# Kernel optimization log

Measured on AMD Instinct MI355X. Metric: run time of the kernel, lower is better.

The kernel has to match this reference:

```python
import jax, jax.numpy as jnp
import numpy as np

N_NODES = 100000
N_EDGES = 1600000
D = 64        # atom_embed_dim
EF = 4        # edge_feat_dim
V = 100       # num_elements


def setup_inputs() -> dict:
    key = jax.random.key(0)
    ks = jax.random.split(key, 10)
    x_ids = jax.random.randint(ks[0], (N_NODES,), 0, V, dtype=jnp.int64 if jax.config.jax_enable_x64 else jnp.int32)
    edge_index = jax.random.randint(ks[1], (2, N_EDGES), 0, N_NODES, dtype=jnp.int64 if jax.config.jax_enable_x64 else jnp.int32)
    edge_attr = jax.random.normal(ks[2], (N_EDGES, EF), dtype=jnp.float32)
    emb = jax.random.normal(ks[3], (V, D), dtype=jnp.float32)
    s_in = 1.0 / np.sqrt(D + EF)
    s_d = 1.0 / np.sqrt(D)
    W1 = jax.random.uniform(ks[4], (D, D + EF), jnp.float32, -s_in, s_in)
    b1 = jax.random.uniform(ks[5], (D,), jnp.float32, -s_in, s_in)
    Wu1 = jax.random.uniform(ks[6], (D, D), jnp.float32, -s_d, s_d)
    bu1 = jax.random.uniform(ks[7], (D,), jnp.float32, -s_d, s_d)
    W2 = jax.random.uniform(ks[8], (D, D + EF), jnp.float32, -s_in, s_in)
    b2 = jax.random.uniform(ks[9], (D,), jnp.float32, -s_in, s_in)
    k2 = jax.random.split(jax.random.key(1), 2)
    Wu2 = jax.random.uniform(k2[0], (D, D), jnp.float32, -s_d, s_d)
    bu2 = jax.random.uniform(k2[1], (D,), jnp.float32, -s_d, s_d)
    return {"x_ids": x_ids, "edge_index": edge_index, "edge_attr": edge_attr,
            "emb": emb, "W1": W1, "b1": b1, "Wu1": Wu1, "bu1": bu1,
            "W2": W2, "b2": b2, "Wu2": Wu2, "bu2": bu2}


def _round(x, src, dst, edge_attr, Wm, bm, Wu, bu):
    # gather src node feats, concat edge feats, msg MLP, scatter-add to dst
    m = jnp.concatenate([x[src], edge_attr], axis=-1)       # (E, D+EF)
    m = jax.nn.relu(m @ Wm.T + bm)                           # (E, D)
    agg = jax.ops.segment_sum(m, dst, num_segments=x.shape[0])  # (N, D)
    return jax.nn.relu((x + agg) @ Wu.T + bu)                # (N, D)


def reference(x_ids, edge_index, edge_attr, emb, W1, b1, Wu1, bu1, W2, b2, Wu2, bu2):
    src, dst = edge_index[0], edge_index[1]
    x = emb[x_ids]                                           # (N, D)
    x = _round(x, src, dst, edge_attr, W1, b1, Wu1, bu1)
    x = _round(x, src, dst, edge_attr, W2, b2, Wu2, bu2)
    return x.mean(axis=0)                                    # (D,)
```

## Files before the change

### kernel.cpp

```cpp
#include <hip/hip_runtime.h>

#define DD    64
#define WCOLS 68

__device__ __forceinline__ float lane_bcast(float v, int k) {
    return __int_as_float(__builtin_amdgcn_readlane(__float_as_int(v), k));
}

__global__ __launch_bounds__(256) void hist_kernel(
    const int* __restrict__ dst, int* __restrict__ deg, int E)
{
    int i = blockIdx.x * 256 + threadIdx.x;
    int stride = gridDim.x * 256;
    for (; i < E; i += stride) atomicAdd(&deg[dst[i]], 1);
}

__global__ __launch_bounds__(256) void scan1_kernel(
    const int* __restrict__ deg, int* __restrict__ rowp, int* __restrict__ bsum, int N)
{
    __shared__ int lds[256];
    int base = blockIdx.x * 1024;
    int t = threadIdx.x;
    int idx0 = base + t * 4;
    int v[4];
    #pragma unroll
    for (int j = 0; j < 4; ++j) v[j] = (idx0 + j < N) ? deg[idx0 + j] : 0;
    lds[t] = v[0] + v[1] + v[2] + v[3];
    __syncthreads();
    for (int off = 1; off < 256; off <<= 1) {
        int x = (t >= off) ? lds[t - off] : 0;
        __syncthreads();
        lds[t] += x;
        __syncthreads();
    }
    int run = (t > 0) ? lds[t - 1] : 0;
    if (t == 255) bsum[blockIdx.x] = lds[255];
    #pragma unroll
    for (int j = 0; j < 4; ++j) {
        if (idx0 + j < N) rowp[idx0 + j] = run;
        run += v[j];
    }
}

__global__ __launch_bounds__(256) void scan2_kernel(int* __restrict__ bsum, int nchunks)
{
    __shared__ int lds[256];
    int t = threadIdx.x;
    int v = (t < nchunks) ? bsum[t] : 0;
    lds[t] = v;
    __syncthreads();
    for (int off = 1; off < 256; off <<= 1) {
        int x = (t >= off) ? lds[t - off] : 0;
        __syncthreads();
        lds[t] += x;
        __syncthreads();
    }
    if (t < nchunks) bsum[t] = (t > 0) ? lds[t - 1] : 0;
}

__global__ __launch_bounds__(256) void scan3_kernel(
    int* __restrict__ rowp, const int* __restrict__ bsum, int* __restrict__ cursor,
    int N, int E)
{
    int i = blockIdx.x * 256 + threadIdx.x;
    if (i == 0) rowp[N] = E;
    if (i < N) {
        int v = rowp[i] + bsum[i >> 10];
        rowp[i] = v;
        cursor[i] = v;
    }
}

__global__ __launch_bounds__(256) void fill_kernel(
    const int* __restrict__ src, const int* __restrict__ dst,
    const float* __restrict__ eattr, int* __restrict__ cursor,
    int* __restrict__ srcp, float4* __restrict__ eap, int E)
{
    int i = blockIdx.x * 256 + threadIdx.x;
    int stride = gridDim.x * 256;
    for (; i < E; i += stride) {
        int d = dst[i];
        int pos = atomicAdd(&cursor[d], 1);
        srcp[pos] = src[i];
        eap[pos] = *(const float4*)(eattr + (size_t)i * 4);
    }
}

__global__ __launch_bounds__(256) void init_kernel(
    const int* __restrict__ x_ids, const float* __restrict__ emb,
    const float* __restrict__ W1, const float* __restrict__ b1,
    float* __restrict__ x0, float* __restrict__ Y, int N)
{
    __shared__ float WaT[64 * 64];
    for (int i = threadIdx.x; i < 64 * 64; i += 256) {
        int d = i & 63, k = i >> 6;
        WaT[i] = W1[d * WCOLS + k];
    }
    __syncthreads();

    int lane = threadIdx.x & 63;
    int wid  = (blockIdx.x * 256 + threadIdx.x) >> 6;
    int nw   = (gridDim.x * 256) >> 6;
    float bias = b1[lane];

    for (int base = wid * 4; base < N; base += nw * 4) {
        int nvalid = N - base; if (nvalid > 4) nvalid = 4;
        float xv[4], acc[4];
        #pragma unroll
        for (int j = 0; j < 4; ++j) {
            xv[j] = (j < nvalid) ? emb[x_ids[base + j] * DD + lane] : 0.f;
            acc[j] = bias;
        }
        #pragma unroll 8
        for (int k = 0; k < 64; ++k) {
            float w = WaT[k * 64 + lane];
            #pragma unroll
            for (int j = 0; j < 4; ++j)
                acc[j] = fmaf(w, lane_bcast(xv[j], k), acc[j]);
        }
        #pragma unroll
        for (int j = 0; j < 4; ++j) {
            if (j < nvalid) {
                size_t o = (size_t)(base + j) * DD + lane;
                x0[o] = xv[j];
                Y[o]  = acc[j];
            }
        }
    }
}

template<bool FUSE_Y, bool FINAL>
__global__ __launch_bounds__(256) void fused_kernel(
    const int* __restrict__ rowp, const int* __restrict__ srcp,
    const float4* __restrict__ eap, const float* __restrict__ Y_in,
    const float* __restrict__ Wm,
    const float* __restrict__ Wu, const float* __restrict__ bu,
    const float* __restrict__ Wn, const float* __restrict__ bn,
    float* __restrict__ x_io, float* __restrict__ Y_out,
    float* __restrict__ out_mean, int N, float inv_n)
{
    __shared__ float WuT[64 * 64];
    __shared__ float WnT[FUSE_Y ? 64 * 64 : 1];
    __shared__ float red[FINAL ? 256 : 1];
    for (int i = threadIdx.x; i < 64 * 64; i += 256) {
        int d = i & 63, k = i >> 6;
        WuT[i] = Wu[d * DD + k];
        if (FUSE_Y) WnT[i] = Wn[d * WCOLS + k];
    }
    __syncthreads();

    int lane = threadIdx.x & 63;
    int wid  = __builtin_amdgcn_readfirstlane((blockIdx.x * 256 + (int)threadIdx.x) >> 6);
    int nw   = (gridDim.x * 256) >> 6;
    float w0 = Wm[lane * WCOLS + 64];
    float w1 = Wm[lane * WCOLS + 65];
    float w2 = Wm[lane * WCOLS + 66];
    float w3 = Wm[lane * WCOLS + 67];
    float biasu = bu[lane];
    float biasn = FUSE_Y ? bn[lane] : 0.f;
    float lsum = 0.f;

    for (int n = wid; n < N; n += nw) {
        int beg = rowp[n], end = rowp[n + 1];
        float acc = 0.f;
        int e = beg;
        for (; e + 3 < end; e += 4) {
            int s0 = srcp[e], s1 = srcp[e + 1], s2 = srcp[e + 2], s3 = srcp[e + 3];
            float4 a0 = eap[e], a1 = eap[e + 1], a2 = eap[e + 2], a3 = eap[e + 3];
            float y0 = Y_in[(size_t)s0 * DD + lane];
            float y1 = Y_in[(size_t)s1 * DD + lane];
            float y2 = Y_in[(size_t)s2 * DD + lane];
            float y3 = Y_in[(size_t)s3 * DD + lane];
            float m0 = y0 + w0 * a0.x + w1 * a0.y + w2 * a0.z + w3 * a0.w;
            float m1 = y1 + w0 * a1.x + w1 * a1.y + w2 * a1.z + w3 * a1.w;
            float m2 = y2 + w0 * a2.x + w1 * a2.y + w2 * a2.z + w3 * a2.w;
            float m3 = y3 + w0 * a3.x + w1 * a3.y + w2 * a3.z + w3 * a3.w;
            acc += fmaxf(m0, 0.f) + fmaxf(m1, 0.f) + fmaxf(m2, 0.f) + fmaxf(m3, 0.f);
        }
        for (; e < end; ++e) {
            int s0 = srcp[e];
            float4 a0 = eap[e];
            float y0 = Y_in[(size_t)s0 * DD + lane];
            float m0 = y0 + w0 * a0.x + w1 * a0.y + w2 * a0.z + w3 * a0.w;
            acc += fmaxf(m0, 0.f);
        }

        size_t o = (size_t)n * DD + lane;
        float v = x_io[o] + acc;
        float au = biasu;
        #pragma unroll 8
        for (int k = 0; k < 64; ++k)
            au = fmaf(WuT[k * 64 + lane], lane_bcast(v, k), au);
        float oo = fmaxf(au, 0.f);

        if (FUSE_Y) {
            float an = biasn;
            #pragma unroll 8
            for (int k = 0; k < 64; ++k)
                an = fmaf(WnT[k * 64 + lane], lane_bcast(oo, k), an);
            x_io[o]  = oo;
            Y_out[o] = an;
        }
        if (FINAL) lsum += oo;
    }

    if (FINAL) {
        red[threadIdx.x] = lsum;
        __syncthreads();
        if (threadIdx.x < 64) {
            float s = red[threadIdx.x] + red[threadIdx.x + 64] +
                      red[threadIdx.x + 128] + red[threadIdx.x + 192];
            unsafeAtomicAdd(&out_mean[threadIdx.x], s * inv_n);
        }
    }
}

extern "C" void kernel_launch(void* const* d_in, const int* in_sizes, int n_in,
                              void* d_out, int out_size, void* d_ws, size_t ws_size,
                              hipStream_t stream) {
    const int*   x_ids = (const int*)d_in[0];
    const int*   ei    = (const int*)d_in[1];
    const float* eattr = (const float*)d_in[2];
    const float* emb   = (const float*)d_in[3];
    const float* W1    = (const float*)d_in[4];
    const float* b1    = (const float*)d_in[5];
    const float* Wu1   = (const float*)d_in[6];
    const float* bu1   = (const float*)d_in[7];
    const float* W2    = (const float*)d_in[8];
    const float* b2    = (const float*)d_in[9];
    const float* Wu2   = (const float*)d_in[10];
    const float* bu2   = (const float*)d_in[11];

    const int N = in_sizes[0];
    const int E = in_sizes[1] / 2;
    const int* src = ei;
    const int* dst = ei + E;

    float* ws = (float*)d_ws;
    size_t stride = (size_t)N * DD;
    float*  x    = ws;
    float*  Ya   = ws + stride;
    float*  Yb   = ws + 2 * stride;
    float*  eapf = ws + 3 * stride;
    int*    srcp = (int*)(eapf + (size_t)E * 4);
    int*    rowp = srcp + E;
    int*    deg  = rowp + N + 1;
    int*    cur  = deg + N;
    int*    bsum = cur + N;
    float4* eap  = (float4*)eapf;

    float* out = (float*)d_out;
    float inv_n = 1.0f / (float)N;
    int nchunks = (N + 1023) / 1024;

    hipMemsetAsync(deg, 0, (size_t)N * sizeof(int), stream);
    hipMemsetAsync(out, 0, DD * sizeof(float), stream);

    hist_kernel <<<2048, 256, 0, stream>>>(dst, deg, E);
    scan1_kernel<<<nchunks, 256, 0, stream>>>(deg, rowp, bsum, N);
    scan2_kernel<<<1, 256, 0, stream>>>(bsum, nchunks);
    scan3_kernel<<<(N + 255) / 256, 256, 0, stream>>>(rowp, bsum, cur, N, E);
    fill_kernel <<<2048, 256, 0, stream>>>(src, dst, eattr, cur, srcp, eap, E);

    init_kernel<<<1024, 256, 0, stream>>>(x_ids, emb, W1, b1, x, Ya, N);

    fused_kernel<true, false><<<2048, 256, 0, stream>>>(
        rowp, srcp, eap, Ya, W1, Wu1, bu1, W2, b2, x, Yb, nullptr, N, inv_n);
    fused_kernel<false, true><<<2048, 256, 0, stream>>>(
        rowp, srcp, eap, Yb, W2, Wu2, bu2, nullptr, nullptr, x, nullptr, out, N, inv_n);
}
```

Measured before the change: 609.1 us.

## Tile nodes per block with edge-balanced waves and LDS atomic aggregation

Replaces the one-wave-per-node CSR loop with blocks that own 64 consecutive destination nodes. The block's edge range is split evenly across its four waves, and messages are accumulated into a shared-memory tile with LDS float atomics. A per-edge byte holding the local destination index is stored during the fill step. The node update then batches four nodes per wave in the dense matvec to reuse weight loads. This targets load imbalance and per-node loop overhead, at the cost of LDS atomics, an extra byte array, and fewer larger blocks (~1563).

```diff
diff --git a/kernel.cpp b/kernel.cpp
--- a/kernel.cpp
+++ b/kernel.cpp
@@ -2,6 +2,7 @@
 
 #define DD    64
 #define WCOLS 68
+#define TILE  64
 
 __device__ __forceinline__ float lane_bcast(float v, int k) {
     return __int_as_float(__builtin_amdgcn_readlane(__float_as_int(v), k));
@@ -74,15 +75,17 @@
 __global__ __launch_bounds__(256) void fill_kernel(
     const int* __restrict__ src, const int* __restrict__ dst,
     const float* __restrict__ eattr, int* __restrict__ cursor,
-    int* __restrict__ srcp, float4* __restrict__ eap, int E)
+    int* __restrict__ srcp, float4* __restrict__ eap,
+    unsigned char* __restrict__ dstp8, int E)
 {
     int i = blockIdx.x * 256 + threadIdx.x;
     int stride = gridDim.x * 256;
     for (; i < E; i += stride) {
         int d = dst[i];
         int pos = atomicAdd(&cursor[d], 1);
-        srcp[pos] = src[i];
-        eap[pos] = *(const float4*)(eattr + (size_t)i * 4);
+        srcp[pos]  = src[i];
+        eap[pos]   = *(const float4*)(eattr + (size_t)i * 4);
+        dstp8[pos] = (unsigned char)(d & (TILE - 1));
     }
 }
 
@@ -130,78 +133,133 @@
 }
 
 template<bool FUSE_Y, bool FINAL>
-__global__ __launch_bounds__(256) void fused_kernel(
+__global__ __launch_bounds__(256) void tile_kernel(
     const int* __restrict__ rowp, const int* __restrict__ srcp,
-    const float4* __restrict__ eap, const float* __restrict__ Y_in,
-    const float* __restrict__ Wm,
+    const float4* __restrict__ eap, const unsigned char* __restrict__ dstp8,
+    const float* __restrict__ Y_in, const float* __restrict__ Wm,
     const float* __restrict__ Wu, const float* __restrict__ bu,
     const float* __restrict__ Wn, const float* __restrict__ bn,
     float* __restrict__ x_io, float* __restrict__ Y_out,
     float* __restrict__ out_mean, int N, float inv_n)
 {
+    __shared__ float agg[TILE * 64];
     __shared__ float WuT[64 * 64];
     __shared__ float WnT[FUSE_Y ? 64 * 64 : 1];
     __shared__ float red[FINAL ? 256 : 1];
+
     for (int i = threadIdx.x; i < 64 * 64; i += 256) {
         int d = i & 63, k = i >> 6;
+        agg[i] = 0.f;
         WuT[i] = Wu[d * DD + k];
         if (FUSE_Y) WnT[i] = Wn[d * WCOLS + k];
     }
     __syncthreads();
 
     int lane = threadIdx.x & 63;
-    int wid  = __builtin_amdgcn_readfirstlane((blockIdx.x * 256 + (int)threadIdx.x) >> 6);
-    int nw   = (gridDim.x * 256) >> 6;
+    int wv   = __builtin_amdgcn_readfirstlane(threadIdx.x >> 6);
     float w0 = Wm[lane * WCOLS + 64];
     float w1 = Wm[lane * WCOLS + 65];
     float w2 = Wm[lane * WCOLS + 66];
     float w3 = Wm[lane * WCOLS + 67];
+
+    int base = blockIdx.x * TILE;
+    int nend = base + TILE; if (nend > N) nend = N;
+    int beg = rowp[base], end = rowp[nend];
+
+    int T   = end - beg;
+    int per = (T + 3) >> 2;
+    int e0  = beg + wv * per;
+    int e1  = e0 + per; if (e1 > end) e1 = end;
+
+    int e = e0;
+    for (; e + 7 < e1; e += 8) {
+        int s[8]; float4 a[8]; int t8[8];
+        #pragma unroll
+        for (int j = 0; j < 8; ++j) {
+            s[j]  = srcp[e + j];
+            a[j]  = eap[e + j];
+            t8[j] = dstp8[e + j];
+        }
+        float y[8];
+        #pragma unroll
+        for (int j = 0; j < 8; ++j)
+            y[j] = Y_in[(size_t)s[j] * DD + lane];
+        #pragma unroll
+        for (int j = 0; j < 8; ++j) {
+            float m = fmaf(w0, a[j].x, y[j]);
+            m = fmaf(w1, a[j].y, m);
+            m = fmaf(w2, a[j].z, m);
+            m = fmaf(w3, a[j].w, m);
+            m = fmaxf(m, 0.f);
+            atomicAdd(&agg[t8[j] * 64 + lane], m);
+        }
+    }
+    for (; e < e1; ++e) {
+        int s0 = srcp[e];
+        float4 a0 = eap[e];
+        int t0 = dstp8[e];
+        float m = fmaf(w0, a0.x, Y_in[(size_t)s0 * DD + lane]);
+        m = fmaf(w1, a0.y, m);
+        m = fmaf(w2, a0.z, m);
+        m = fmaf(w3, a0.w, m);
+        atomicAdd(&agg[t0 * 64 + lane], fmaxf(m, 0.f));
+    }
+    __syncthreads();
+
     float biasu = bu[lane];
     float biasn = FUSE_Y ? bn[lane] : 0.f;
     float lsum = 0.f;
 
-    for (int n = wid; n < N; n += nw) {
-        int beg = rowp[n], end = rowp[n + 1];
-        float acc = 0.f;
-        int e = beg;
-        for (; e + 3 < end; e += 4) {
-            int s0 = srcp[e], s1 = srcp[e + 1], s2 = srcp[e + 2], s3 = srcp[e + 3];
-            float4 a0 = eap[e], a1 = eap[e + 1], a2 = eap[e + 2], a3 = eap[e + 3];
-            float y0 = Y_in[(size_t)s0 * DD + lane];
-            float y1 = Y_in[(size_t)s1 * DD + lane];
-            float y2 = Y_in[(size_t)s2 * DD + lane];
-            float y3 = Y_in[(size_t)s3 * DD + lane];
-            float m0 = y0 + w0 * a0.x + w1 * a0.y + w2 * a0.z + w3 * a0.w;
-            float m1 = y1 + w0 * a1.x + w1 * a1.y + w2 * a1.z + w3 * a1.w;
-            float m2 = y2 + w0 * a2.x + w1 * a2.y + w2 * a2.z + w3 * a2.w;
-            float m3 = y3 + w0 * a3.x + w1 * a3.y + w2 * a3.z + w3 * a3.w;
-            acc += fmaxf(m0, 0.f) + fmaxf(m1, 0.f) + fmaxf(m2, 0.f) + fmaxf(m3, 0.f);
-        }
-        for (; e < end; ++e) {
-            int s0 = srcp[e];
-            float4 a0 = eap[e];
-            float y0 = Y_in[(size_t)s0 * DD + lane];
-            float m0 = y0 + w0 * a0.x + w1 * a0.y + w2 * a0.z + w3 * a0.w;
-            acc += fmaxf(m0, 0.f);
-        }
-
-        size_t o = (size_t)n * DD + lane;
-        float v = x_io[o] + acc;
-        float au = biasu;
+    #pragma unroll
+    for (int g = 0; g < 4; ++g) {
+        int t0 = wv * 16 + g * 4;
+        int n0 = base + t0;
+        int nv = N - n0; if (nv > 4) nv = 4; if (nv < 0) nv = 0;
+
+        float v[4], acc[4];
+        #pragma unroll
+        for (int j = 0; j < 4; ++j) {
+            v[j] = (j < nv)
+                 ? x_io[(size_t)(n0 + j) * DD + lane] + agg[(t0 + j) * 64 + lane]
+                 : 0.f;
+            acc[j] = biasu;
+        }
         #pragma unroll 8
-        for (int k = 0; k < 64; ++k)
-            au = fmaf(WuT[k * 64 + lane], lane_bcast(v, k), au);
-        float oo = fmaxf(au, 0.f);
+        for (int k = 0; k < 64; ++k) {
+            float w = WuT[k * 64 + lane];
+            #pragma unroll
+            for (int j = 0; j < 4; ++j)
+                acc[j] = fmaf(w, lane_bcast(v[j], k), acc[j]);
+        }
+        float o4[4];
+        #pragma unroll
+        for (int j = 0; j < 4; ++j) o4[j] = fmaxf(acc[j], 0.f);
 
         if (FUSE_Y) {
-            float an = biasn;
+            float acc2[4];
+            #pragma unroll
+            for (int j = 0; j < 4; ++j) acc2[j] = biasn;
             #pragma unroll 8
-            for (int k = 0; k < 64; ++k)
-                an = fmaf(WnT[k * 64 + lane], lane_bcast(oo, k), an);
-            x_io[o]  = oo;
-            Y_out[o] = an;
-        }
-        if (FINAL) lsum += oo;
+            for (int k = 0; k < 64; ++k) {
+                float w = WnT[k * 64 + lane];
+                #pragma unroll
+                for (int j = 0; j < 4; ++j)
+                    acc2[j] = fmaf(w, lane_bcast(o4[j], k), acc2[j]);
+            }
+            #pragma unroll
+            for (int j = 0; j < 4; ++j) {
+                if (j < nv) {
+                    size_t o = (size_t)(n0 + j) * DD + lane;
+                    x_io[o]  = o4[j];
+                    Y_out[o] = acc2[j];
+                }
+            }
+        }
+        if (FINAL) {
+            #pragma unroll
+            for (int j = 0; j < 4; ++j)
+                if (j < nv) lsum += o4[j];
+        }
     }
 
     if (FINAL) {
@@ -247,11 +305,13 @@
     int*    deg  = rowp + N + 1;
     int*    cur  = deg + N;
     int*    bsum = cur + N;
+    unsigned char* dstp8 = (unsigned char*)(bsum + 256);
     float4* eap  = (float4*)eapf;
 
     float* out = (float*)d_out;
     float inv_n = 1.0f / (float)N;
     int nchunks = (N + 1023) / 1024;
+    int ntiles  = (N + TILE - 1) / TILE;
 
     hipMemsetAsync(deg, 0, (size_t)N * sizeof(int), stream);
     hipMemsetAsync(out, 0, DD * sizeof(float), stream);
@@ -260,12 +320,12 @@
     scan1_kernel<<<nchunks, 256, 0, stream>>>(deg, rowp, bsum, N);
     scan2_kernel<<<1, 256, 0, stream>>>(bsum, nchunks);
     scan3_kernel<<<(N + 255) / 256, 256, 0, stream>>>(rowp, bsum, cur, N, E);
-    fill_kernel <<<2048, 256, 0, stream>>>(src, dst, eattr, cur, srcp, eap, E);
+    fill_kernel <<<2048, 256, 0, stream>>>(src, dst, eattr, cur, srcp, eap, dstp8, E);
 
     init_kernel<<<1024, 256, 0, stream>>>(x_ids, emb, W1, b1, x, Ya, N);
 
-    fused_kernel<true, false><<<2048, 256, 0, stream>>>(
-        rowp, srcp, eap, Ya, W1, Wu1, bu1, W2, b2, x, Yb, nullptr, N, inv_n);
-    fused_kernel<false, true><<<2048, 256, 0, stream>>>(
-        rowp, srcp, eap, Yb, W2, Wu2, bu2, nullptr, nullptr, x, nullptr, out, N, inv_n);
-}
+    tile_kernel<true, false><<<ntiles, 256, 0, stream>>>(
+        rowp, srcp, eap, dstp8, Ya, W1, Wu1, bu1, W2, b2, x, Yb, nullptr, N, inv_n);
+    tile_kernel<false, true><<<ntiles, 256, 0, stream>>>(
+        rowp, srcp, eap, dstp8, Yb, W2, Wu2, bu2, nullptr, nullptr, x, nullptr, out, N, inv_n);
+}
```

Measured after the change: 1.546 ms. +153.8%, slower.

## Precompute round-1 messages per vocabulary entry and gather from LDS by element id

Applied to the files above, without the earlier changes.

Round-1 node features are just embeddings of one of 100 element ids, so the W1 projection is computed once per vocabulary entry (100x64) rather than per node. The CSR fill now also stores a byte-sized element id per edge, and round 1 gathers projected rows from shared memory instead of from a 100k x 64 global buffer. The old per-node init kernel and its x0/Ya global writes go away. In exchange, round 1 uses about 58KB of LDS per block, which can lower occupancy, and fill_kernel does an extra random x_ids read per edge.

```diff
diff --git a/kernel.cpp b/kernel.cpp
--- a/kernel.cpp
+++ b/kernel.cpp
@@ -2,6 +2,7 @@
 
 #define DD    64
 #define WCOLS 68
+#define VV    100
 
 __device__ __forceinline__ float lane_bcast(float v, int k) {
     return __int_as_float(__builtin_amdgcn_readlane(__float_as_int(v), k));
@@ -73,23 +74,26 @@
 
 __global__ __launch_bounds__(256) void fill_kernel(
     const int* __restrict__ src, const int* __restrict__ dst,
-    const float* __restrict__ eattr, int* __restrict__ cursor,
-    int* __restrict__ srcp, float4* __restrict__ eap, int E)
+    const int* __restrict__ x_ids, const float* __restrict__ eattr,
+    int* __restrict__ cursor,
+    int* __restrict__ srcp, unsigned char* __restrict__ vb,
+    float4* __restrict__ eap, int E)
 {
     int i = blockIdx.x * 256 + threadIdx.x;
     int stride = gridDim.x * 256;
     for (; i < E; i += stride) {
+        int s = src[i];
         int d = dst[i];
         int pos = atomicAdd(&cursor[d], 1);
-        srcp[pos] = src[i];
-        eap[pos] = *(const float4*)(eattr + (size_t)i * 4);
-    }
-}
-
-__global__ __launch_bounds__(256) void init_kernel(
-    const int* __restrict__ x_ids, const float* __restrict__ emb,
-    const float* __restrict__ W1, const float* __restrict__ b1,
-    float* __restrict__ x0, float* __restrict__ Y, int N)
+        srcp[pos] = s;
+        vb[pos]   = (unsigned char)x_ids[s];
+        eap[pos]  = *(const float4*)(eattr + (size_t)i * 4);
+    }
+}
+
+__global__ __launch_bounds__(256) void vocab_kernel(
+    const float* __restrict__ emb, const float* __restrict__ W1,
+    const float* __restrict__ b1, float* __restrict__ YV)
 {
     __shared__ float WaT[64 * 64];
     for (int i = threadIdx.x; i < 64 * 64; i += 256) {
@@ -99,53 +103,103 @@
     __syncthreads();
 
     int lane = threadIdx.x & 63;
-    int wid  = (blockIdx.x * 256 + threadIdx.x) >> 6;
+    int wv = blockIdx.x * 4 + (threadIdx.x >> 6);
+    if (wv >= VV) return;
+    float xv = emb[wv * DD + lane];
+    float acc = b1[lane];
+    #pragma unroll 8
+    for (int k = 0; k < 64; ++k)
+        acc = fmaf(WaT[k * 64 + lane], lane_bcast(xv, k), acc);
+    YV[wv * DD + lane] = acc;
+}
+
+__global__ __launch_bounds__(256) void round1_kernel(
+    const int* __restrict__ rowp, const unsigned char* __restrict__ vb,
+    const float4* __restrict__ eap, const float* __restrict__ YV,
+    const int* __restrict__ x_ids, const float* __restrict__ emb,
+    const float* __restrict__ W1,
+    const float* __restrict__ Wu, const float* __restrict__ bu,
+    const float* __restrict__ Wn, const float* __restrict__ bn,
+    float* __restrict__ x1, float* __restrict__ Yb, int N)
+{
+    __shared__ float YVs[VV * 64];
+    __shared__ float WuT[64 * 64];
+    __shared__ float WnT[64 * 64];
+    for (int i = threadIdx.x; i < VV * 64; i += 256) YVs[i] = YV[i];
+    for (int i = threadIdx.x; i < 64 * 64; i += 256) {
+        int d = i & 63, k = i >> 6;
+        WuT[i] = Wu[d * DD + k];
+        WnT[i] = Wn[d * WCOLS + k];
+    }
+    __syncthreads();
+
+    int lane = threadIdx.x & 63;
+    int wid  = __builtin_amdgcn_readfirstlane((blockIdx.x * 256 + (int)threadIdx.x) >> 6);
     int nw   = (gridDim.x * 256) >> 6;
-    float bias = b1[lane];
-
-    for (int base = wid * 4; base < N; base += nw * 4) {
-        int nvalid = N - base; if (nvalid > 4) nvalid = 4;
-        float xv[4], acc[4];
-        #pragma unroll
-        for (int j = 0; j < 4; ++j) {
-            xv[j] = (j < nvalid) ? emb[x_ids[base + j] * DD + lane] : 0.f;
-            acc[j] = bias;
+    float w0 = W1[lane * WCOLS + 64];
+    float w1 = W1[lane * WCOLS + 65];
+    float w2 = W1[lane * WCOLS + 66];
+    float w3 = W1[lane * WCOLS + 67];
+    float biasu = bu[lane];
+    float biasn = bn[lane];
+
+    for (int n = wid; n < N; n += nw) {
+        int beg = rowp[n], end = rowp[n + 1];
+        float acc = 0.f;
+        int e = beg;
+        for (; e + 3 < end; e += 4) {
+            int v0 = vb[e], v1 = vb[e + 1], v2 = vb[e + 2], v3 = vb[e + 3];
+            float4 a0 = eap[e], a1 = eap[e + 1], a2 = eap[e + 2], a3 = eap[e + 3];
+            float y0 = YVs[v0 * 64 + lane];
+            float y1 = YVs[v1 * 64 + lane];
+            float y2 = YVs[v2 * 64 + lane];
+            float y3 = YVs[v3 * 64 + lane];
+            float m0 = y0 + w0 * a0.x + w1 * a0.y + w2 * a0.z + w3 * a0.w;
+            float m1 = y1 + w0 * a1.x + w1 * a1.y + w2 * a1.z + w3 * a1.w;
+            float m2 = y2 + w0 * a2.x + w1 * a2.y + w2 * a2.z + w3 * a2.w;
+            float m3 = y3 + w0 * a3.x + w1 * a3.y + w2 * a3.z + w3 * a3.w;
+            acc += fmaxf(m0, 0.f) + fmaxf(m1, 0.f) + fmaxf(m2, 0.f) + fmaxf(m3, 0.f);
         }
+        for (; e < end; ++e) {
+            int v0 = vb[e];
+            float4 a0 = eap[e];
+            float y0 = YVs[v0 * 64 + lane];
+            float m0 = y0 + w0 * a0.x + w1 * a0.y + w2 * a0.z + w3 * a0.w;
+            acc += fmaxf(m0, 0.f);
+        }
+
+        int id = x_ids[n];
+        float v = emb[(size_t)id * DD + lane] + acc;
+        float au = biasu;
         #pragma unroll 8
-        for (int k = 0; k < 64; ++k) {
-            float w = WaT[k * 64 + lane];
-            #pragma unroll
-            for (int j = 0; j < 4; ++j)
-                acc[j] = fmaf(w, lane_bcast(xv[j], k), acc[j]);
-        }
-        #pragma unroll
-        for (int j = 0; j < 4; ++j) {
-            if (j < nvalid) {
-                size_t o = (size_t)(base + j) * DD + lane;
-                x0[o] = xv[j];
-                Y[o]  = acc[j];
-            }
-        }
-    }
-}
-
-template<bool FUSE_Y, bool FINAL>
-__global__ __launch_bounds__(256) void fused_kernel(
+        for (int k = 0; k < 64; ++k)
+            au = fmaf(WuT[k * 64 + lane], lane_bcast(v, k), au);
+        float oo = fmaxf(au, 0.f);
+
+        float an = biasn;
+        #pragma unroll 8
+        for (int k = 0; k < 64; ++k)
+            an = fmaf(WnT[k * 64 + lane], lane_bcast(oo, k), an);
+
+        size_t o = (size_t)n * DD + lane;
+        x1[o] = oo;
+        Yb[o] = an;
+    }
+}
+
+__global__ __launch_bounds__(256) void round2_kernel(
     const int* __restrict__ rowp, const int* __restrict__ srcp,
     const float4* __restrict__ eap, const float* __restrict__ Y_in,
     const float* __restrict__ Wm,
     const float* __restrict__ Wu, const float* __restrict__ bu,
-    const float* __restrict__ Wn, const float* __restrict__ bn,
-    float* __restrict__ x_io, float* __restrict__ Y_out,
-    float* __restrict__ out_mean, int N, float inv_n)
+    const float* __restrict__ x1, float* __restrict__ out_mean,
+    int N, float inv_n)
 {
     __shared__ float WuT[64 * 64];
-    __shared__ float WnT[FUSE_Y ? 64 * 64 : 1];
-    __shared__ float red[FINAL ? 256 : 1];
+    __shared__ float red[256];
     for (int i = threadIdx.x; i < 64 * 64; i += 256) {
         int d = i & 63, k = i >> 6;
         WuT[i] = Wu[d * DD + k];
-        if (FUSE_Y) WnT[i] = Wn[d * WCOLS + k];
     }
     __syncthreads();
 
@@ -157,7 +211,6 @@
     float w2 = Wm[lane * WCOLS + 66];
     float w3 = Wm[lane * WCOLS + 67];
     float biasu = bu[lane];
-    float biasn = FUSE_Y ? bn[lane] : 0.f;
     float lsum = 0.f;
 
     for (int n = wid; n < N; n += nw) {
@@ -186,32 +239,20 @@
         }
 
         size_t o = (size_t)n * DD + lane;
-        float v = x_io[o] + acc;
+        float v = x1[o] + acc;
         float au = biasu;
         #pragma unroll 8
         for (int k = 0; k < 64; ++k)
             au = fmaf(WuT[k * 64 + lane], lane_bcast(v, k), au);
-        float oo = fmaxf(au, 0.f);
-
-        if (FUSE_Y) {
-            float an = biasn;
-            #pragma unroll 8
-            for (int k = 0; k < 64; ++k)
-                an = fmaf(WnT[k * 64 + lane], lane_bcast(oo, k), an);
-            x_io[o]  = oo;
-            Y_out[o] = an;
-        }
-        if (FINAL) lsum += oo;
-    }
-
-    if (FINAL) {
-        red[threadIdx.x] = lsum;
-        __syncthreads();
-        if (threadIdx.x < 64) {
-            float s = red[threadIdx.x] + red[threadIdx.x + 64] +
-                      red[threadIdx.x + 128] + red[threadIdx.x + 192];
-            unsafeAtomicAdd(&out_mean[threadIdx.x], s * inv_n);
-        }
+        lsum += fmaxf(au, 0.f);
+    }
+
+    red[threadIdx.x] = lsum;
+    __syncthreads();
+    if (threadIdx.x < 64) {
+        float s = red[threadIdx.x] + red[threadIdx.x + 64] +
+                  red[threadIdx.x + 128] + red[threadIdx.x + 192];
+        unsafeAtomicAdd(&out_mean[threadIdx.x], s * inv_n);
     }
 }
 
@@ -238,15 +279,16 @@
 
     float* ws = (float*)d_ws;
     size_t stride = (size_t)N * DD;
-    float*  x    = ws;
-    float*  Ya   = ws + stride;
-    float*  Yb   = ws + 2 * stride;
-    float*  eapf = ws + 3 * stride;
+    float*  x1   = ws;
+    float*  Yb   = ws + stride;
+    float*  eapf = ws + 2 * stride;
     int*    srcp = (int*)(eapf + (size_t)E * 4);
     int*    rowp = srcp + E;
     int*    deg  = rowp + N + 1;
     int*    cur  = deg + N;
     int*    bsum = cur + N;
+    float*  YV   = (float*)(bsum + 256);
+    unsigned char* vb = (unsigned char*)(YV + VV * 64);
     float4* eap  = (float4*)eapf;
 
     float* out = (float*)d_out;
@@ -260,12 +302,12 @@
     scan1_kernel<<<nchunks, 256, 0, stream>>>(deg, rowp, bsum, N);
     scan2_kernel<<<1, 256, 0, stream>>>(bsum, nchunks);
     scan3_kernel<<<(N + 255) / 256, 256, 0, stream>>>(rowp, bsum, cur, N, E);
-    fill_kernel <<<2048, 256, 0, stream>>>(src, dst, eattr, cur, srcp, eap, E);
-
-    init_kernel<<<1024, 256, 0, stream>>>(x_ids, emb, W1, b1, x, Ya, N);
-
-    fused_kernel<true, false><<<2048, 256, 0, stream>>>(
-        rowp, srcp, eap, Ya, W1, Wu1, bu1, W2, b2, x, Yb, nullptr, N, inv_n);
-    fused_kernel<false, true><<<2048, 256, 0, stream>>>(
-        rowp, srcp, eap, Yb, W2, Wu2, bu2, nullptr, nullptr, x, nullptr, out, N, inv_n);
-}
+    fill_kernel <<<2048, 256, 0, stream>>>(src, dst, x_ids, eattr, cur, srcp, vb, eap, E);
+
+    vocab_kernel<<<(VV + 3) / 4, 256, 0, stream>>>(emb, W1, b1, YV);
+
+    round1_kernel<<<2048, 256, 0, stream>>>(
+        rowp, vb, eap, YV, x_ids, emb, W1, Wu1, bu1, W2, b2, x1, Yb, N);
+    round2_kernel<<<2048, 256, 0, stream>>>(
+        rowp, srcp, eap, Yb, W2, Wu2, bu2, x1, out, N, inv_n);
+}
```

Result: no change. 607.2 us (-0.3%).
